# Kernel optimization log

Hardware: AMD Instinct MI355X
Metric: run time of the kernel (lower is better)

Reference implementation:

```python
import jax, jax.numpy as jnp
import numpy as np

N_OBJ, N_REL = 16384, 32768
HID, POOL = 512, 4096
N_OBJ_CLS, N_REL_CLS = 151, 51


def setup_inputs() -> dict:
    key = jax.random.key(0)
    ks = jax.random.split(key, 12)
    return {
        "edge_ctx": jax.random.normal(ks[0], (N_OBJ, HID), jnp.float32),
        "union_features": jax.random.normal(ks[1], (N_REL, POOL), jnp.float32),
        "pair_idx": jax.random.randint(ks[2], (N_REL, 2), 0, N_OBJ, jnp.int64) if jax.config.jax_enable_x64 else jax.random.randint(ks[2], (N_REL, 2), 0, N_OBJ, jnp.int32),
        "obj_preds": jax.random.randint(ks[3], (N_OBJ,), 0, N_OBJ_CLS, jnp.int32),
        "W_post_emb": jax.random.normal(ks[4], (2 * HID, HID), jnp.float32) * (10.0 / np.sqrt(HID)),
        "b_post_emb": jax.random.normal(ks[5], (2 * HID,), jnp.float32) * 0.01,
        "W_post_cat": jax.random.normal(ks[6], (POOL, 2 * HID), jnp.float32) * (1.0 / np.sqrt(2 * HID)),
        "b_post_cat": jax.random.normal(ks[7], (POOL,), jnp.float32) * 0.01,
        "W_rel": jax.random.normal(ks[8], (N_REL_CLS, POOL), jnp.float32) * (1.0 / np.sqrt(POOL)),
        "b_rel": jax.random.normal(ks[9], (N_REL_CLS,), jnp.float32) * 0.01,
        "freq_bias": jax.random.normal(ks[10], (N_OBJ_CLS, N_OBJ_CLS, N_REL_CLS), jnp.float32),
    }


def reference(edge_ctx, union_features, pair_idx, obj_preds,
              W_post_emb, b_post_emb, W_post_cat, b_post_cat,
              W_rel, b_rel, freq_bias):
    # post_emb: [N_obj, H] -> [N_obj, 2H] -> head/tail reps [N_obj, H]
    edge_rep = edge_ctx @ W_post_emb.T + b_post_emb            # [N_obj, 2H]
    edge_rep = edge_rep.reshape(edge_rep.shape[0], 2, HID)
    head_rep = edge_rep[:, 0]                                  # [N_obj, H]
    tail_rep = edge_rep[:, 1]                                  # [N_obj, H]

    h_idx = pair_idx[:, 0]
    t_idx = pair_idx[:, 1]
    # gather + concat head/tail pair features -> [N_rel, 2H]
    prod_rep = jnp.concatenate([head_rep[h_idx], tail_rep[t_idx]], axis=-1)
    # post_cat linear -> [N_rel, POOL]
    prod_rep = prod_rep @ W_post_cat.T + b_post_cat
    # use_vision, pooling_dim == MLP_HEAD_DIM -> elementwise product
    prod_rep = prod_rep * union_features
    # rel_compress -> [N_rel, num_rel_cls]
    rel_dists = prod_rep @ W_rel.T + b_rel
    # frequency bias lookup indexed by (head class, tail class)
    bias = freq_bias[obj_preds[h_idx], obj_preds[t_idx]]       # [N_rel, num_rel_cls]
    return rel_dists + bias
```

## Files before the change

kernel.cpp:

```cpp
#include <hip/hip_runtime.h>

#define N_OBJ 16384
#define N_REL 32768
#define HID 512
#define POOL 4096
#define NCLS 151
#define NRELCLS 51

#define AS1 __attribute__((address_space(1)))
#define AS3 __attribute__((address_space(3)))

#define LDSSZ 131072

typedef __attribute__((ext_vector_type(8))) short short8;
typedef __attribute__((ext_vector_type(4))) float f32x4;

__device__ __forceinline__ unsigned short f2bf(float x) {
    unsigned u = __float_as_uint(x);
    u += 0x7fff + ((u >> 16) & 1);
    return (unsigned short)(u >> 16);
}

__global__ void cvt_kernel(const float* __restrict__ in, unsigned short* __restrict__ out, long n8) {
    long i = (long)blockIdx.x * blockDim.x + threadIdx.x;
    if (i >= n8) return;
    const float4* p = (const float4*)in;
    float4 a = p[2 * i], b = p[2 * i + 1];
    short8 o;
    o[0] = f2bf(a.x); o[1] = f2bf(a.y); o[2] = f2bf(a.z); o[3] = f2bf(a.w);
    o[4] = f2bf(b.x); o[5] = f2bf(b.y); o[6] = f2bf(b.z); o[7] = f2bf(b.w);
    ((short8*)out)[i] = o;
}

__global__ void cvt_wrel_kernel(const float* __restrict__ W, unsigned short* __restrict__ out) {
    int gid = blockIdx.x * 256 + threadIdx.x;
    int row = gid >> 9;
    int c8 = (gid & 511) << 3;
    short8 o = {};
    if (row < NRELCLS) {
        const float* src = W + (long)row * POOL + c8;
        float4 a = *(const float4*)src, b = *(const float4*)(src + 4);
        o[0] = f2bf(a.x); o[1] = f2bf(a.y); o[2] = f2bf(a.z); o[3] = f2bf(a.w);
        o[4] = f2bf(b.x); o[5] = f2bf(b.y); o[6] = f2bf(b.z); o[7] = f2bf(b.w);
    }
    *(short8*)(out + (long)row * POOL + c8) = o;
}

__device__ __forceinline__ void stage_tile128x64(const unsigned short* __restrict__ src,
                                                 unsigned short* lds,
                                                 int row0, int rowStrideElems, int col0,
                                                 int wave, int lane) {
    const char* s = (const char*)(src + (long)row0 * rowStrideElems + col0);
    long strideB = (long)rowStrideElems * 2;
#pragma unroll
    for (int is = 0; is < 4; ++is) {
        int issue = wave * 4 + is;
        const char* g = s + (long)(issue * 8 + (lane >> 3)) * strideB + (lane & 7) * 16;
        __builtin_amdgcn_global_load_lds((const AS1 void*)g,
                                         (AS3 void*)((char*)lds + issue * 1024),
                                         16, 0, 0);
    }
}

__global__ __launch_bounds__(256) void gemm1_kernel(const unsigned short* __restrict__ A,
                                                    const unsigned short* __restrict__ B,
                                                    const float* __restrict__ bias,
                                                    unsigned short* __restrict__ C) {
    __shared__ __align__(16) unsigned short At[128 * 64];
    __shared__ __align__(16) unsigned short Bt[128 * 64];
    int row0 = blockIdx.x * 128, col0 = blockIdx.y * 128;
    int tid = threadIdx.x, wave = tid >> 6, lane = tid & 63;
    int wr = (wave >> 1) * 64, wc = (wave & 1) * 64;
    int lrow = lane & 15, lko = (lane >> 4) * 8;
    f32x4 acc[4][4] = {};
    for (int kt = 0; kt < HID / 64; ++kt) {
        stage_tile128x64(A, At, row0, HID, kt * 64, wave, lane);
        stage_tile128x64(B, Bt, col0, HID, kt * 64, wave, lane);
        __syncthreads();
#pragma unroll
        for (int ks = 0; ks < 2; ++ks) {
            short8 af[4], bf[4];
#pragma unroll
            for (int mi = 0; mi < 4; ++mi) af[mi] = *(const short8*)(At + (wr + 16 * mi + lrow) * 64 + ks * 32 + lko);
#pragma unroll
            for (int ni = 0; ni < 4; ++ni) bf[ni] = *(const short8*)(Bt + (wc + 16 * ni + lrow) * 64 + ks * 32 + lko);
#pragma unroll
            for (int mi = 0; mi < 4; ++mi)
#pragma unroll
                for (int ni = 0; ni < 4; ++ni)
                    acc[mi][ni] = __builtin_amdgcn_mfma_f32_16x16x32_bf16(af[mi], bf[ni], acc[mi][ni], 0, 0, 0);
        }
        __syncthreads();
    }
#pragma unroll
    for (int mi = 0; mi < 4; ++mi)
#pragma unroll
        for (int ni = 0; ni < 4; ++ni)
#pragma unroll
            for (int i = 0; i < 4; ++i) {
                int r = row0 + wr + 16 * mi + 4 * (lane >> 4) + i;
                int c = col0 + wc + 16 * ni + lrow;
                C[(long)r * 1024 + c] = f2bf(acc[mi][ni][i] + bias[c]);
            }
}

__global__ __launch_bounds__(512) void reduce_kernel(const float* __restrict__ part,
                                                     const int* __restrict__ pair_idx,
                                                     const int* __restrict__ obj_preds,
                                                     const float* __restrict__ b_rel,
                                                     const float* __restrict__ freq_bias,
                                                     float* __restrict__ out) {
    int r = blockIdx.x * 8 + (threadIdx.x >> 6);
    int lane = threadIdx.x & 63;
    if (lane < NRELCLS) {
        int h = pair_idx[2 * r], t = pair_idx[2 * r + 1];
        long fidx = ((long)obj_preds[h] * NCLS + obj_preds[t]) * NRELCLS + lane;
        float s = b_rel[lane] + freq_bias[fidx];
#pragma unroll
        for (int p = 0; p < 16; ++p)
            s += part[((long)p * N_REL + r) * NRELCLS + lane];
        out[(long)r * NRELCLS + lane] = s;
    }
}

__device__ __forceinline__ void stage_half(const char* __restrict__ erepb, const char* __restrict__ Wcb,
                                           char* lds, int slot, int t, int i0, int col0,
                                           const int* hA, const int* tA,
                                           const int* arowA, const int* colbA, int w) {
    int kb = t * 128;
    int head = (kb < 1024);
#pragma unroll
    for (int i = i0; i < i0 + 2; ++i) {
        int obase = i * 8192 + w * 1024;
        int idx = head ? hA[i] : tA[i];
        __builtin_amdgcn_global_load_lds((const AS1 void*)(erepb + (long)idx * 2048 + kb + colbA[i]),
                                         (AS3 void*)(lds + slot * 32768 + obase), 16, 0, 0);
        __builtin_amdgcn_global_load_lds((const AS1 void*)(Wcb + (long)(col0 + arowA[i]) * 2048 + kb + colbA[i]),
                                         (AS3 void*)(lds + 65536 + slot * 32768 + obase), 16, 0, 0);
    }
}

__device__ __forceinline__ void read_bfrags(const char* B, int wc, int lrow, int lcb, short8 bF[4][2]) {
#pragma unroll
    for (int ni = 0; ni < 4; ++ni)
#pragma unroll
        for (int ks = 0; ks < 2; ++ks) {
            int r = wc + 16 * ni + lrow;
            bF[ni][ks] = *(const short8*)(B + r * 128 + ((ks * 64 + lcb) ^ ((r & 7) << 4)));
        }
}

__device__ __forceinline__ void read_afrags(const char* A, int p, int wr, int lrow, int lcb, short8 aF[2][2]) {
#pragma unroll
    for (int m = 0; m < 2; ++m)
#pragma unroll
        for (int ks = 0; ks < 2; ++ks) {
            int r = wr + 16 * (2 * p + m) + lrow;
            aF[m][ks] = *(const short8*)(A + r * 128 + ((ks * 64 + lcb) ^ ((r & 7) << 4)));
        }
}

__device__ __forceinline__ void mfma16(int p, short8 aF[2][2], short8 bF[4][2], f32x4 acc[8][4]) {
    __builtin_amdgcn_s_setprio(1);
#pragma unroll
    for (int m = 0; m < 2; ++m)
#pragma unroll
        for (int ni = 0; ni < 4; ++ni)
#pragma unroll
            for (int ks = 0; ks < 2; ++ks)
                acc[2 * p + m][ni] = __builtin_amdgcn_mfma_f32_16x16x32_bf16(aF[m][ks], bF[ni][ks], acc[2 * p + m][ni], 0, 0, 0);
    __builtin_amdgcn_s_setprio(0);
}

__global__ __launch_bounds__(512, 1) void fused_kernel(
    const unsigned short* __restrict__ erep,
    const unsigned short* __restrict__ Wcat,
    const unsigned short* __restrict__ Wrelp,
    const float* __restrict__ unionf,
    const float* __restrict__ bcat,
    const int* __restrict__ pair_idx,
    float* __restrict__ part) {
    __shared__ __align__(16) char lds[LDSSZ];
    int bid = blockIdx.x;
    int xcd = bid & 7, j = bid >> 3;
    int panel = (xcd << 1) | (j >> 7);
    int row0 = (j & 127) * 256, col0 = panel * 256;
    int tid = threadIdx.x, w = tid >> 6, lane = tid & 63;
    int wr = (w >> 2) * 128, wc = (w & 3) * 64;
    int lrow = lane & 15, lcb = (lane >> 4) * 16;
    const char* erepb = (const char*)erep;
    const char* Wcb = (const char*)Wcat;
    f32x4 acc2[8][4] = {};

    int hA[4], tA[4], arowA[4], colbA[4];
#pragma unroll
    for (int i = 0; i < 4; ++i) {
        int o = i * 8192 + w * 1024 + lane * 16;
        int ar = o >> 7, cin = o & 127;
        arowA[i] = ar;
        colbA[i] = cin ^ ((ar & 7) << 4);
        hA[i] = pair_idx[2 * (row0 + ar)];
        tA[i] = pair_idx[2 * (row0 + ar) + 1];
    }

    stage_half(erepb, Wcb, lds, 0, 0, 0, col0, hA, tA, arowA, colbA, w);
    stage_half(erepb, Wcb, lds, 0, 0, 2, col0, hA, tA, arowA, colbA, w);

    for (int t = 0; t < 16; ++t) {
        const char* A = lds + (t & 1) * 32768;
        const char* B = lds + 65536 + (t & 1) * 32768;
        int sn = (t + 1) & 1;
        short8 bF[4][2];
#pragma unroll
        for (int p = 0; p < 4; ++p) {
            short8 aF[2][2];
            if (p == 0) {
                if (t < 15) {
                    stage_half(erepb, Wcb, lds, sn, t + 1, 0, col0, hA, tA, arowA, colbA, w);
                    asm volatile("s_waitcnt vmcnt(4)" ::: "memory");
                } else {
                    asm volatile("s_waitcnt vmcnt(0)" ::: "memory");
                }
                __builtin_amdgcn_s_barrier();
                __builtin_amdgcn_sched_barrier(0);
                read_bfrags(B, wc, lrow, lcb, bF);
                read_afrags(A, 0, wr, lrow, lcb, aF);
            } else {
                read_afrags(A, p, wr, lrow, lcb, aF);
                if (p == 2 && t < 15)
                    stage_half(erepb, Wcb, lds, sn, t + 1, 2, col0, hA, tA, arowA, colbA, w);
                __builtin_amdgcn_s_barrier();
                __builtin_amdgcn_sched_barrier(0);
            }
            asm volatile("s_waitcnt lgkmcnt(0)" ::: "memory");
            __builtin_amdgcn_sched_barrier(0);
            mfma16(p, aF, bF, acc2);
            __builtin_amdgcn_s_barrier();
        }
    }

    asm volatile("s_waitcnt lgkmcnt(0)" ::: "memory");
    __builtin_amdgcn_sched_barrier(0);
    __builtin_amdgcn_s_barrier();
    __builtin_amdgcn_sched_barrier(0);

    {
        float bcv[4];
#pragma unroll
        for (int ni = 0; ni < 4; ++ni) bcv[ni] = bcat[col0 + wc + 16 * ni + lrow];
#pragma unroll
        for (int mi = 0; mi < 8; ++mi)
#pragma unroll
            for (int ni = 0; ni < 4; ++ni) {
                int pcol = wc + 16 * ni + lrow;
#pragma unroll
                for (int i = 0; i < 4; ++i) {
                    int prow = wr + 16 * mi + 4 * (lane >> 4) + i;
                    float u = __builtin_nontemporal_load(
                        &unionf[(long)(row0 + prow) * 4096 + col0 + pcol]);
                    *(unsigned short*)(lds + prow * 512 + ((pcol * 2) ^ ((prow & 7) << 4)))
                        = f2bf((acc2[mi][ni][i] + bcv[ni]) * u);
                }
            }
    }
    asm volatile("s_waitcnt lgkmcnt(0)" ::: "memory");
    __builtin_amdgcn_sched_barrier(0);
    __builtin_amdgcn_s_barrier();
    __builtin_amdgcn_sched_barrier(0);

    f32x4 acc3[2][4] = {};
    const char* Wrb = (const char*)Wrelp;
#pragma unroll
    for (int ks = 0; ks < 8; ++ks) {
        int cb2 = ks * 64 + lcb;
        short8 wb[4], pa[2];
#pragma unroll
        for (int ni = 0; ni < 4; ++ni) {
            int r2 = 16 * ni + lrow;
            wb[ni] = *(const short8*)(Wrb + (long)r2 * 8192 + col0 * 2 + cb2);
        }
#pragma unroll
        for (int mi = 0; mi < 2; ++mi) {
            int r2 = w * 32 + 16 * mi + lrow;
            pa[mi] = *(const short8*)(lds + r2 * 512 + (cb2 ^ ((r2 & 7) << 4)));
        }
#pragma unroll
        for (int mi = 0; mi < 2; ++mi)
#pragma unroll
            for (int ni = 0; ni < 4; ++ni)
                acc3[mi][ni] = __builtin_amdgcn_mfma_f32_16x16x32_bf16(pa[mi], wb[ni], acc3[mi][ni], 0, 0, 0);
    }
#pragma unroll
    for (int mi = 0; mi < 2; ++mi)
#pragma unroll
        for (int ni = 0; ni < 4; ++ni)
#pragma unroll
            for (int i = 0; i < 4; ++i) {
                int r = row0 + w * 32 + 16 * mi + 4 * (lane >> 4) + i;
                int cc = 16 * ni + lrow;
                if (cc < NRELCLS)
                    part[((long)panel * N_REL + r) * NRELCLS + cc] = acc3[mi][ni][i];
            }
}

extern "C" void kernel_launch(void* const* d_in, const int* in_sizes, int n_in,
                              void* d_out, int out_size, void* d_ws, size_t ws_size,
                              hipStream_t stream) {
    const float* edge_ctx  = (const float*)d_in[0];
    const float* unionf    = (const float*)d_in[1];
    const int*   pair_idx  = (const int*)d_in[2];
    const int*   obj_preds = (const int*)d_in[3];
    const float* W_emb     = (const float*)d_in[4];
    const float* b_emb     = (const float*)d_in[5];
    const float* W_cat     = (const float*)d_in[6];
    const float* b_cat     = (const float*)d_in[7];
    const float* W_rel     = (const float*)d_in[8];
    const float* b_rel     = (const float*)d_in[9];
    const float* freq_bias = (const float*)d_in[10];
    float* out = (float*)d_out;

    char* ws = (char*)d_ws;
    unsigned short* ecb   = (unsigned short*)ws; ws += (size_t)N_OBJ * HID * 2;
    unsigned short* Wembb = (unsigned short*)ws; ws += (size_t)1024 * HID * 2;
    unsigned short* Wcatb = (unsigned short*)ws; ws += (size_t)POOL * 1024 * 2;
    unsigned short* Wrelb = (unsigned short*)ws; ws += (size_t)64 * POOL * 2;
    unsigned short* erep  = (unsigned short*)ws; ws += (size_t)N_OBJ * 1024 * 2;
    float*          part  = (float*)ws;          ws += (size_t)16 * N_REL * NRELCLS * 4;

    cvt_kernel<<<4096, 256, 0, stream>>>(edge_ctx, ecb, (long)N_OBJ * HID / 8);
    cvt_kernel<<<256, 256, 0, stream>>>(W_emb, Wembb, (long)1024 * HID / 8);
    cvt_kernel<<<2048, 256, 0, stream>>>(W_cat, Wcatb, (long)POOL * 1024 / 8);
    cvt_wrel_kernel<<<128, 256, 0, stream>>>(W_rel, Wrelb);
    gemm1_kernel<<<dim3(128, 8), 256, 0, stream>>>(ecb, Wembb, b_emb, erep);
    fused_kernel<<<2048, 512, 0, stream>>>(erep, Wcatb, Wrelb, unionf, b_cat, pair_idx, part);
    reduce_kernel<<<4096, 512, 0, stream>>>(part, pair_idx, obj_preds, b_rel, freq_bias, out);
}
```

Measured before the change: 466.4 us.

## Shrink fused GEMM tile to 128x256 with 256-thread blocks, two per CU

The fused gather+GEMM kernel moves from a 256x256 tile with 8 waves and 128 KB of LDS to a 128x256 tile with 4 waves and 64 KB of LDS, so two blocks can share a CU. The K step is halved to 32 elements and the double-buffered pipeline is reorganised: the B tile is staged before the first MFMA half and the gathered A tile between the two halves, with a 4-way XOR swizzle. The aim is more latency hiding through block-level concurrency and lower per-block LDS and register pressure. In exchange, data reuse per tile drops and the weight panel is re-read twice as often, with more barriers per unit of work.

```diff
diff --git a/kernel.cpp b/kernel.cpp
--- a/kernel.cpp
+++ b/kernel.cpp
@@ -10,7 +10,7 @@
 #define AS1 __attribute__((address_space(1)))
 #define AS3 __attribute__((address_space(3)))
 
-#define LDSSZ 131072
+#define LDSSZ 65536
 
 typedef __attribute__((ext_vector_type(8))) short short8;
 typedef __attribute__((ext_vector_type(4))) float f32x4;
@@ -123,56 +123,34 @@
     }
 }
 
-__device__ __forceinline__ void stage_half(const char* __restrict__ erepb, const char* __restrict__ Wcb,
-                                           char* lds, int slot, int t, int i0, int col0,
-                                           const int* hA, const int* tA,
-                                           const int* arowA, const int* colbA, int w) {
-    int kb = t * 128;
+__device__ __forceinline__ void stage_B(const char* __restrict__ Wcb, char* lds, int s, int t,
+                                        int col0, int w, int lane) {
+    int kb = t * 64;
+#pragma unroll
+    for (int i = 0; i < 4; ++i) {
+        int obase = i * 4096 + w * 1024;
+        int o = obase + lane * 16;
+        int row = o >> 6, cin = o & 63;
+        int c = cin ^ ((row & 3) << 4);
+        __builtin_amdgcn_global_load_lds((const AS1 void*)(Wcb + (long)(col0 + row) * 2048 + kb + c),
+                                         (AS3 void*)(lds + 16384 + s * 16384 + obase), 16, 0, 0);
+    }
+}
+
+__device__ __forceinline__ void stage_A(const char* __restrict__ erepb, char* lds, int s, int t,
+                                        const int* hA, const int* tA, const int* colbA, int w) {
+    int kb = t * 64;
     int head = (kb < 1024);
 #pragma unroll
-    for (int i = i0; i < i0 + 2; ++i) {
-        int obase = i * 8192 + w * 1024;
+    for (int i = 0; i < 2; ++i) {
+        int obase = i * 4096 + w * 1024;
         int idx = head ? hA[i] : tA[i];
         __builtin_amdgcn_global_load_lds((const AS1 void*)(erepb + (long)idx * 2048 + kb + colbA[i]),
-                                         (AS3 void*)(lds + slot * 32768 + obase), 16, 0, 0);
-        __builtin_amdgcn_global_load_lds((const AS1 void*)(Wcb + (long)(col0 + arowA[i]) * 2048 + kb + colbA[i]),
-                                         (AS3 void*)(lds + 65536 + slot * 32768 + obase), 16, 0, 0);
-    }
-}
-
-__device__ __forceinline__ void read_bfrags(const char* B, int wc, int lrow, int lcb, short8 bF[4][2]) {
-#pragma unroll
-    for (int ni = 0; ni < 4; ++ni)
-#pragma unroll
-        for (int ks = 0; ks < 2; ++ks) {
-            int r = wc + 16 * ni + lrow;
-            bF[ni][ks] = *(const short8*)(B + r * 128 + ((ks * 64 + lcb) ^ ((r & 7) << 4)));
-        }
-}
-
-__device__ __forceinline__ void read_afrags(const char* A, int p, int wr, int lrow, int lcb, short8 aF[2][2]) {
-#pragma unroll
-    for (int m = 0; m < 2; ++m)
-#pragma unroll
-        for (int ks = 0; ks < 2; ++ks) {
-            int r = wr + 16 * (2 * p + m) + lrow;
-            aF[m][ks] = *(const short8*)(A + r * 128 + ((ks * 64 + lcb) ^ ((r & 7) << 4)));
-        }
-}
-
-__device__ __forceinline__ void mfma16(int p, short8 aF[2][2], short8 bF[4][2], f32x4 acc[8][4]) {
-    __builtin_amdgcn_s_setprio(1);
-#pragma unroll
-    for (int m = 0; m < 2; ++m)
-#pragma unroll
-        for (int ni = 0; ni < 4; ++ni)
-#pragma unroll
-            for (int ks = 0; ks < 2; ++ks)
-                acc[2 * p + m][ni] = __builtin_amdgcn_mfma_f32_16x16x32_bf16(aF[m][ks], bF[ni][ks], acc[2 * p + m][ni], 0, 0, 0);
-    __builtin_amdgcn_s_setprio(0);
-}
-
-__global__ __launch_bounds__(512, 1) void fused_kernel(
+                                         (AS3 void*)(lds + s * 8192 + obase), 16, 0, 0);
+    }
+}
+
+__global__ __launch_bounds__(256, 2) void fused_kernel(
     const unsigned short* __restrict__ erep,
     const unsigned short* __restrict__ Wcat,
     const unsigned short* __restrict__ Wrelp,
@@ -183,60 +161,79 @@
     __shared__ __align__(16) char lds[LDSSZ];
     int bid = blockIdx.x;
     int xcd = bid & 7, j = bid >> 3;
-    int panel = (xcd << 1) | (j >> 7);
-    int row0 = (j & 127) * 256, col0 = panel * 256;
+    int panel = (xcd << 1) | (j >> 8);
+    int row0 = (j & 255) * 128, col0 = panel * 256;
     int tid = threadIdx.x, w = tid >> 6, lane = tid & 63;
-    int wr = (w >> 2) * 128, wc = (w & 3) * 64;
+    int wr = (w >> 1) * 64, wc = (w & 1) * 128;
     int lrow = lane & 15, lcb = (lane >> 4) * 16;
     const char* erepb = (const char*)erep;
     const char* Wcb = (const char*)Wcat;
-    f32x4 acc2[8][4] = {};
-
-    int hA[4], tA[4], arowA[4], colbA[4];
-#pragma unroll
-    for (int i = 0; i < 4; ++i) {
-        int o = i * 8192 + w * 1024 + lane * 16;
-        int ar = o >> 7, cin = o & 127;
-        arowA[i] = ar;
-        colbA[i] = cin ^ ((ar & 7) << 4);
+    f32x4 acc2[4][8] = {};
+
+    int hA[2], tA[2], colbA[2];
+#pragma unroll
+    for (int i = 0; i < 2; ++i) {
+        int o = i * 4096 + w * 1024 + lane * 16;
+        int ar = o >> 6, cin = o & 63;
+        colbA[i] = cin ^ ((ar & 3) << 4);
         hA[i] = pair_idx[2 * (row0 + ar)];
         tA[i] = pair_idx[2 * (row0 + ar) + 1];
     }
 
-    stage_half(erepb, Wcb, lds, 0, 0, 0, col0, hA, tA, arowA, colbA, w);
-    stage_half(erepb, Wcb, lds, 0, 0, 2, col0, hA, tA, arowA, colbA, w);
-
-    for (int t = 0; t < 16; ++t) {
-        const char* A = lds + (t & 1) * 32768;
-        const char* B = lds + 65536 + (t & 1) * 32768;
+    stage_B(Wcb, lds, 0, 0, col0, w, lane);
+    stage_A(erepb, lds, 0, 0, hA, tA, colbA, w);
+
+    for (int t = 0; t < 32; ++t) {
+        const char* A = lds + (t & 1) * 8192;
+        const char* B = lds + 16384 + (t & 1) * 16384;
         int sn = (t + 1) & 1;
-        short8 bF[4][2];
-#pragma unroll
-        for (int p = 0; p < 4; ++p) {
-            short8 aF[2][2];
-            if (p == 0) {
-                if (t < 15) {
-                    stage_half(erepb, Wcb, lds, sn, t + 1, 0, col0, hA, tA, arowA, colbA, w);
-                    asm volatile("s_waitcnt vmcnt(4)" ::: "memory");
-                } else {
-                    asm volatile("s_waitcnt vmcnt(0)" ::: "memory");
-                }
-                __builtin_amdgcn_s_barrier();
-                __builtin_amdgcn_sched_barrier(0);
-                read_bfrags(B, wc, lrow, lcb, bF);
-                read_afrags(A, 0, wr, lrow, lcb, aF);
-            } else {
-                read_afrags(A, p, wr, lrow, lcb, aF);
-                if (p == 2 && t < 15)
-                    stage_half(erepb, Wcb, lds, sn, t + 1, 2, col0, hA, tA, arowA, colbA, w);
-                __builtin_amdgcn_s_barrier();
-                __builtin_amdgcn_sched_barrier(0);
-            }
-            asm volatile("s_waitcnt lgkmcnt(0)" ::: "memory");
-            __builtin_amdgcn_sched_barrier(0);
-            mfma16(p, aF, bF, acc2);
-            __builtin_amdgcn_s_barrier();
-        }
+        short8 aF[4], bF[4];
+        if (t < 31) {
+            stage_B(Wcb, lds, sn, t + 1, col0, w, lane);
+            asm volatile("s_waitcnt vmcnt(4)" ::: "memory");
+        } else {
+            asm volatile("s_waitcnt vmcnt(0)" ::: "memory");
+        }
+        __builtin_amdgcn_s_barrier();
+        __builtin_amdgcn_sched_barrier(0);
+#pragma unroll
+        for (int m = 0; m < 4; ++m) {
+            int r = wr + 16 * m + lrow;
+            aF[m] = *(const short8*)(A + r * 64 + (lcb ^ ((r & 3) << 4)));
+        }
+#pragma unroll
+        for (int ni = 0; ni < 4; ++ni) {
+            int r = wc + 16 * ni + lrow;
+            bF[ni] = *(const short8*)(B + r * 64 + (lcb ^ ((r & 3) << 4)));
+        }
+        asm volatile("s_waitcnt lgkmcnt(0)" ::: "memory");
+        __builtin_amdgcn_sched_barrier(0);
+        __builtin_amdgcn_s_setprio(1);
+#pragma unroll
+        for (int m = 0; m < 4; ++m)
+#pragma unroll
+            for (int ni = 0; ni < 4; ++ni)
+                acc2[m][ni] = __builtin_amdgcn_mfma_f32_16x16x32_bf16(aF[m], bF[ni], acc2[m][ni], 0, 0, 0);
+        __builtin_amdgcn_s_setprio(0);
+        __builtin_amdgcn_s_barrier();
+#pragma unroll
+        for (int ni = 0; ni < 4; ++ni) {
+            int r = wc + 16 * (ni + 4) + lrow;
+            bF[ni] = *(const short8*)(B + r * 64 + (lcb ^ ((r & 3) << 4)));
+        }
+        if (t < 31) stage_A(erepb, lds, sn, t + 1, hA, tA, colbA, w);
+        __builtin_amdgcn_s_barrier();
+        __builtin_amdgcn_sched_barrier(0);
+        asm volatile("s_waitcnt lgkmcnt(0)" ::: "memory");
+        __builtin_amdgcn_sched_barrier(0);
+        __builtin_amdgcn_s_setprio(1);
+#pragma unroll
+        for (int m = 0; m < 4; ++m)
+#pragma unroll
+            for (int ni = 0; ni < 4; ++ni)
+                acc2[m][ni + 4] = __builtin_amdgcn_mfma_f32_16x16x32_bf16(aF[m], bF[ni], acc2[m][ni + 4], 0, 0, 0);
+        __builtin_amdgcn_s_setprio(0);
+        __builtin_amdgcn_s_barrier();
     }
 
     asm volatile("s_waitcnt lgkmcnt(0)" ::: "memory");
@@ -245,13 +242,13 @@
     __builtin_amdgcn_sched_barrier(0);
 
     {
-        float bcv[4];
-#pragma unroll
-        for (int ni = 0; ni < 4; ++ni) bcv[ni] = bcat[col0 + wc + 16 * ni + lrow];
-#pragma unroll
-        for (int mi = 0; mi < 8; ++mi)
-#pragma unroll
-            for (int ni = 0; ni < 4; ++ni) {
+        float bcv[8];
+#pragma unroll
+        for (int ni = 0; ni < 8; ++ni) bcv[ni] = bcat[col0 + wc + 16 * ni + lrow];
+#pragma unroll
+        for (int mi = 0; mi < 4; ++mi)
+#pragma unroll
+            for (int ni = 0; ni < 8; ++ni) {
                 int pcol = wc + 16 * ni + lrow;
 #pragma unroll
                 for (int i = 0; i < 4; ++i) {
@@ -332,6 +329,6 @@
     cvt_kernel<<<2048, 256, 0, stream>>>(W_cat, Wcatb, (long)POOL * 1024 / 8);
     cvt_wrel_kernel<<<128, 256, 0, stream>>>(W_rel, Wrelb);
     gemm1_kernel<<<dim3(128, 8), 256, 0, stream>>>(ecb, Wembb, b_emb, erep);
-    fused_kernel<<<2048, 512, 0, stream>>>(erep, Wcatb, Wrelb, unionf, b_cat, pair_idx, part);
+    fused_kernel<<<4096, 256, 0, stream>>>(erep, Wcatb, Wrelb, unionf, b_cat, pair_idx, part);
     reduce_kernel<<<4096, 512, 0, stream>>>(part, pair_idx, obj_preds, b_rel, freq_bias, out);
 }
```

New measurement: 475.1 us. Within noise of the previous version (+1.9%).
